# Kernel tuning notes

Hardware: AMD Instinct MI355X
Metric: run time of the kernel (lower is better)

Reference implementation:

```python
import jax, jax.numpy as jnp
import numpy as np

N = 50000      # nodes
E = 800000     # edges (avg degree 16)
IN = 512       # input_dim
R = 128        # feat_reduce_dim
F = 64         # hid_dim per head
H = 4          # n_heads
OUT = 64       # output_dim
ALPHA = 0.2    # leaky_relu slope


def setup_inputs() -> dict:
    key = jax.random.key(0)
    ks = jax.random.split(key, 12)
    x = jax.random.normal(ks[0], (N, IN), dtype=jnp.float32)
    edges = jax.random.randint(ks[1], (2, E), 0, N, dtype=jnp.int32)
    # per-head GAT layer params (fan-in scaled so exp(logits) stays finite)
    W_lin_h = jax.random.normal(ks[2], (H, R, IN), dtype=jnp.float32) * (IN ** -0.5)
    W_seq_h = jax.random.normal(ks[3], (H, F, R), dtype=jnp.float32) * (R ** -0.5)
    a1_h = jax.random.normal(ks[4], (H, F), dtype=jnp.float32) * (F ** -0.5)
    b1_h = jnp.zeros((H,), dtype=jnp.float32)
    a2_h = jax.random.normal(ks[5], (H, F), dtype=jnp.float32) * (F ** -0.5)
    b2_h = jnp.zeros((H,), dtype=jnp.float32)
    bias_h = jnp.zeros((H, F), dtype=jnp.float32)
    # classifier GAT layer (in = H*F = 256, out = OUT)
    W_lin_c = jax.random.normal(ks[6], (R, H * F), dtype=jnp.float32) * ((H * F) ** -0.5)
    W_seq_c = jax.random.normal(ks[7], (OUT, R), dtype=jnp.float32) * (R ** -0.5)
    a1_c = jax.random.normal(ks[8], (OUT,), dtype=jnp.float32) * (OUT ** -0.5)
    b1_c = jnp.zeros((), dtype=jnp.float32)
    a2_c = jax.random.normal(ks[9], (OUT,), dtype=jnp.float32) * (OUT ** -0.5)
    b2_c = jnp.zeros((), dtype=jnp.float32)
    bias_c = jnp.zeros((OUT,), dtype=jnp.float32)
    return dict(x=x, edges=edges, W_lin_h=W_lin_h, W_seq_h=W_seq_h, a1_h=a1_h,
                b1_h=b1_h, a2_h=a2_h, b2_h=b2_h, bias_h=bias_h,
                W_lin_c=W_lin_c, W_seq_c=W_seq_c, a1_c=a1_c, b1_c=b1_c,
                a2_c=a2_c, b2_c=b2_c, bias_c=bias_c)


def _gat_layer(x, src, dst, W_lin, W_seq, a1, b1, a2, b2, bias, concat):
    n = x.shape[0]
    h = x @ W_lin.T                    # [N, R]   (Linear, no bias)
    s = h @ W_seq.T                    # [N, F]   (Conv1d k=1 == matmul)
    f1 = s @ a1 + b1                   # [N]      (f_1 conv)
    f2 = s @ a2 + b2                   # [N]      (f_2 conv)
    logits = f1[src] + f2[dst]         # [E]  edge-gather
    coefs = jnp.exp(jax.nn.leaky_relu(logits, ALPHA))          # [E]
    denom = jax.ops.segment_sum(coefs, src, num_segments=n)    # [N]
    agg = jax.ops.segment_sum(coefs[:, None] * s[dst], src, num_segments=n)  # [N, F]
    ret = agg / denom[:, None] + bias
    return jax.nn.elu(ret) if concat else ret


def reference(x, edges, W_lin_h, W_seq_h, a1_h, b1_h, a2_h, b2_h, bias_h,
              W_lin_c, W_seq_c, a1_c, b1_c, a2_c, b2_c, bias_c):
    src, dst = edges[0], edges[1]
    # n_heads attention layers (concat=True), vmapped over the head axis
    heads = jax.vmap(
        lambda Wl, Ws, a1, b1, a2, b2, b: _gat_layer(
            x, src, dst, Wl, Ws, a1, b1, a2, b2, b, True)
    )(W_lin_h, W_seq_h, a1_h, b1_h, a2_h, b2_h, bias_h)        # [H, N, F]
    hcat = jnp.transpose(heads, (1, 0, 2)).reshape(x.shape[0], -1)  # [N, H*F]
    # classifier GAT layer (concat=False -> no ELU)
    out = _gat_layer(hcat, src, dst, W_lin_c, W_seq_c, a1_c, b1_c,
                     a2_c, b2_c, bias_c, False)                # [N, OUT]
    return out
```

## Files before the change

### kernel.cpp

```cpp
#include <hip/hip_runtime.h>
#include <hip/hip_bf16.h>
#include <cstddef>
#include <cstdint>

#define IN_DIM 512
#define R_DIM 128
#define F_DIM 64
#define H_NUM 4
#define OUT_DIM 64
#define HF 256

typedef __attribute__((ext_vector_type(4))) float f32x4;
typedef __attribute__((ext_vector_type(8))) short bf16x8;

typedef const __attribute__((address_space(1))) void gas_void;
typedef __attribute__((address_space(3))) void las_void;

__device__ __forceinline__ float bf2f(ushort u) {
    union { uint i; float f; } v; v.i = ((uint)u) << 16; return v.f;
}
__device__ __forceinline__ ushort f2bf(float f) {
    union { float f; uint i; } v; v.f = f;
    uint r = v.i + 0x7fff + ((v.i >> 16) & 1);
    return (ushort)(r >> 16);
}
__device__ __forceinline__ float u2f(uint u) {
    union { uint i; float f; } v; v.i = u; return v.f;
}

__global__ __launch_bounds__(256) void zero_i32(int* __restrict__ p, int n) {
    int i = blockIdx.x * 256 + threadIdx.x;
    if (i < n) p[i] = 0;
}

__global__ __launch_bounds__(256) void wcomb_kernel(const float* __restrict__ WlinH,
                                                    const float* __restrict__ WseqH,
                                                    const float* __restrict__ WlinC,
                                                    const float* __restrict__ WseqC,
                                                    ushort* __restrict__ Wc1,
                                                    ushort* __restrict__ Wc2) {
    int idx = blockIdx.x * 256 + threadIdx.x;
    if (idx < H_NUM * F_DIM * IN_DIM) {
        int i  = idx & (IN_DIM - 1);
        int hf = idx >> 9;
        int h  = hf >> 6;
        const float* ws = WseqH + (size_t)hf * R_DIM;
        const float* wl = WlinH + (size_t)h * R_DIM * IN_DIM + i;
        float acc = 0.0f;
#pragma unroll 8
        for (int r = 0; r < R_DIM; ++r) acc += ws[r] * wl[(size_t)r * IN_DIM];
        Wc1[idx] = f2bf(acc);
    } else {
        int idx2 = idx - H_NUM * F_DIM * IN_DIM;
        if (idx2 >= OUT_DIM * HF) return;
        int j = idx2 & (HF - 1);
        int o = idx2 >> 8;
        const float* ws = WseqC + (size_t)o * R_DIM;
        const float* wl = WlinC + j;
        float acc = 0.0f;
#pragma unroll 8
        for (int r = 0; r < R_DIM; ++r) acc += ws[r] * wl[(size_t)r * HF];
        Wc2[idx2] = f2bf(acc);
    }
}

template<int BN, int K, int FS>
__global__ __launch_bounds__(256) void gemm_f32a(const float* __restrict__ A,
                                                 const ushort* __restrict__ B,
                                                 ushort* __restrict__ C,
                                                 int M, int Ntot,
                                                 const float* __restrict__ a1,
                                                 const float* __restrict__ b1,
                                                 const float* __restrict__ a2,
                                                 const float* __restrict__ b2,
                                                 float* __restrict__ f1o,
                                                 float* __restrict__ f2o) {
    constexpr int NF = BN / 16;
    constexpr int HH = BN / 64;
    __shared__ ushort As[64 * 64];
    __shared__ ushort Bs[BN * 64];
    const int tid = threadIdx.x;
    const int wave = tid >> 6;
    const int lane = tid & 63;
    const int lr = lane & 15;
    const int lg = lane >> 4;

    const int b = blockIdx.x;
    const int by = (b >> 3) & 1;
    const int bx = (b >> 4) * 8 + (b & 7);
    const int nbx = (M + 63) >> 6;
    if (bx >= nbx) return;
    const int m0 = bx * 64;
    const int n0 = by * BN;
    const int h0 = by * HH;

    int base[2];
#pragma unroll
    for (int ks = 0; ks < 2; ++ks)
        base[ks] = lr * 128 + (((ks * 4 + lg) ^ (lr & 7)) * 16);
    const int abase0 = wave * 2048 + base[0];
    const int abase1 = wave * 2048 + base[1];

    int s_grow[2], s_ldsoff[2], s_goff[2];
#pragma unroll
    for (int r = 0; r < 2; ++r) {
        int off = r * 4096 + tid * 16;
        int row = off >> 7;
        int lchunk = (off >> 4) & 7;
        int grow = m0 + row;
        if (grow >= M) grow = M - 1;
        s_grow[r] = grow;
        s_goff[r] = lchunk * 8;
        s_ldsoff[r] = row * 128 + ((lchunk ^ (row & 7)) * 16);
    }

    f32x4 acc[NF];
#pragma unroll
    for (int cb = 0; cb < NF; ++cb) acc[cb] = (f32x4)0.0f;

    for (int k0 = 0; k0 < K; k0 += 64) {
#pragma unroll
        for (int r = 0; r < BN / 32; ++r) {
            int off = r * 4096 + tid * 16;
            int row = off >> 7;
            int kch = ((off >> 4) & 7) ^ (row & 7);
            const ushort* g = B + (size_t)(n0 + row) * K + k0 + kch * 8;
            __builtin_amdgcn_global_load_lds((gas_void*)g,
                                             (las_void*)((char*)Bs + off), 16, 0, 0);
        }
#pragma unroll
        for (int r = 0; r < 2; ++r) {
            const float* g = A + (size_t)s_grow[r] * K + k0 + s_goff[r];
            float4 v0 = *(const float4*)(g);
            float4 v1 = *(const float4*)(g + 4);
            ushort us[8] = {f2bf(v0.x), f2bf(v0.y), f2bf(v0.z), f2bf(v0.w),
                            f2bf(v1.x), f2bf(v1.y), f2bf(v1.z), f2bf(v1.w)};
            *(uint4*)((char*)As + s_ldsoff[r]) = *(const uint4*)us;
        }
        __syncthreads();
        {
            bf16x8 af0 = *(const bf16x8*)((const char*)As + abase0);
            bf16x8 af1 = *(const bf16x8*)((const char*)As + abase1);
#pragma unroll
            for (int cg = 0; cg < NF / 4; ++cg) {
                bf16x8 bfr[4];
#pragma unroll
                for (int j = 0; j < 4; ++j)
                    bfr[j] = *(const bf16x8*)((const char*)Bs + (cg * 4 + j) * 2048 + base[0]);
#pragma unroll
                for (int j = 0; j < 4; ++j)
                    acc[cg * 4 + j] = __builtin_amdgcn_mfma_f32_16x16x32_bf16(
                        af0, bfr[j], acc[cg * 4 + j], 0, 0, 0);
#pragma unroll
                for (int j = 0; j < 4; ++j)
                    bfr[j] = *(const bf16x8*)((const char*)Bs + (cg * 4 + j) * 2048 + base[1]);
#pragma unroll
                for (int j = 0; j < 4; ++j)
                    acc[cg * 4 + j] = __builtin_amdgcn_mfma_f32_16x16x32_bf16(
                        af1, bfr[j], acc[cg * 4 + j], 0, 0, 0);
            }
        }
        __syncthreads();
    }

    float a1v[NF], a2v[NF];
#pragma unroll
    for (int cb = 0; cb < NF; ++cb) {
        int col = n0 + cb * 16 + lr;
        a1v[cb] = a1[col];
        a2v[cb] = a2[col];
    }
    const int rowb = m0 + wave * 16 + lg * 4;
#pragma unroll
    for (int r = 0; r < 4; ++r) {
        int row = rowb + r;
        bool ok = row < M;
#pragma unroll
        for (int hh = 0; hh < HH; ++hh) {
            float p1 = 0.f, p2 = 0.f;
#pragma unroll
            for (int c4 = 0; c4 < 4; ++c4) {
                int cb = hh * 4 + c4;
                float v = acc[cb][r];
                p1 += v * a1v[cb];
                p2 += v * a2v[cb];
                if (ok) C[(size_t)row * Ntot + n0 + cb * 16 + lr] = f2bf(v);
            }
#pragma unroll
            for (int m = 1; m < 16; m <<= 1) {
                p1 += __shfl_xor(p1, m, 64);
                p2 += __shfl_xor(p2, m, 64);
            }
            if (lr == 0 && ok) {
                f1o[(size_t)row * FS + h0 + hh] = p1 + b1[h0 + hh];
                f2o[(size_t)row * FS + h0 + hh] = p2 + b2[h0 + hh];
            }
        }
    }
}

template<int BN, int K, int FS>
__global__ __launch_bounds__(256) void gemm_bf16(const ushort* __restrict__ A,
                                                 const ushort* __restrict__ B,
                                                 ushort* __restrict__ C,
                                                 int M, int Ntot,
                                                 const float* __restrict__ a1,
                                                 const float* __restrict__ b1,
                                                 const float* __restrict__ a2,
                                                 const float* __restrict__ b2,
                                                 float* __restrict__ f1o,
                                                 float* __restrict__ f2o) {
    constexpr int NF = BN / 16;
    constexpr int HH = BN / 64;
    __shared__ ushort As[64 * 64];
    __shared__ ushort Bs[BN * 64];
    const int tid = threadIdx.x;
    const int wave = tid >> 6;
    const int lane = tid & 63;
    const int lr = lane & 15;
    const int lg = lane >> 4;
    const int m0 = blockIdx.x * 64;

    int base[2];
#pragma unroll
    for (int ks = 0; ks < 2; ++ks)
        base[ks] = lr * 128 + (((ks * 4 + lg) ^ (lr & 7)) * 16);
    const int abase0 = wave * 2048 + base[0];
    const int abase1 = wave * 2048 + base[1];

    f32x4 acc[NF];
#pragma unroll
    for (int cb = 0; cb < NF; ++cb) acc[cb] = (f32x4)0.0f;

    for (int k0 = 0; k0 < K; k0 += 64) {
#pragma unroll
        for (int r = 0; r < 2; ++r) {
            int off = r * 4096 + tid * 16;
            int row = off >> 7;
            int kch = ((off >> 4) & 7) ^ (row & 7);
            const ushort* g = A + (size_t)(m0 + row) * K + k0 + kch * 8;
            __builtin_amdgcn_global_load_lds((gas_void*)g,
                                             (las_void*)((char*)As + off), 16, 0, 0);
        }
#pragma unroll
        for (int r = 0; r < BN / 32; ++r) {
            int off = r * 4096 + tid * 16;
            int row = off >> 7;
            int kch = ((off >> 4) & 7) ^ (row & 7);
            const ushort* g = B + (size_t)row * K + k0 + kch * 8;
            __builtin_amdgcn_global_load_lds((gas_void*)g,
                                             (las_void*)((char*)Bs + off), 16, 0, 0);
        }
        __syncthreads();
        {
            bf16x8 af0 = *(const bf16x8*)((const char*)As + abase0);
            bf16x8 af1 = *(const bf16x8*)((const char*)As + abase1);
#pragma unroll
            for (int cg = 0; cg < NF / 4; ++cg) {
                bf16x8 bfr[4];
#pragma unroll
                for (int j = 0; j < 4; ++j)
                    bfr[j] = *(const bf16x8*)((const char*)Bs + (cg * 4 + j) * 2048 + base[0]);
#pragma unroll
                for (int j = 0; j < 4; ++j)
                    acc[cg * 4 + j] = __builtin_amdgcn_mfma_f32_16x16x32_bf16(
                        af0, bfr[j], acc[cg * 4 + j], 0, 0, 0);
#pragma unroll
                for (int j = 0; j < 4; ++j)
                    bfr[j] = *(const bf16x8*)((const char*)Bs + (cg * 4 + j) * 2048 + base[1]);
#pragma unroll
                for (int j = 0; j < 4; ++j)
                    acc[cg * 4 + j] = __builtin_amdgcn_mfma_f32_16x16x32_bf16(
                        af1, bfr[j], acc[cg * 4 + j], 0, 0, 0);
            }
        }
        __syncthreads();
    }

    float a1v[NF], a2v[NF];
#pragma unroll
    for (int cb = 0; cb < NF; ++cb) {
        int col = cb * 16 + lr;
        a1v[cb] = a1[col];
        a2v[cb] = a2[col];
    }
    const int rowb = m0 + wave * 16 + lg * 4;
#pragma unroll
    for (int r = 0; r < 4; ++r) {
        int row = rowb + r;
        bool ok = row < M;
#pragma unroll
        for (int hh = 0; hh < HH; ++hh) {
            float p1 = 0.f, p2 = 0.f;
#pragma unroll
            for (int c4 = 0; c4 < 4; ++c4) {
                int cb = hh * 4 + c4;
                float v = acc[cb][r];
                p1 += v * a1v[cb];
                p2 += v * a2v[cb];
                if (ok) C[(size_t)row * Ntot + cb * 16 + lr] = f2bf(v);
            }
#pragma unroll
            for (int m = 1; m < 16; m <<= 1) {
                p1 += __shfl_xor(p1, m, 64);
                p2 += __shfl_xor(p2, m, 64);
            }
            if (lr == 0 && ok) {
                f1o[(size_t)row * FS + hh] = p1 + b1[hh];
                f2o[(size_t)row * FS + hh] = p2 + b2[hh];
            }
        }
    }
}

__global__ __launch_bounds__(256) void hist_kernel(const int* __restrict__ src,
                                                   int* __restrict__ counts, int E) {
    int e = blockIdx.x * 256 + threadIdx.x;
    if (e < E) atomicAdd(&counts[src[e]], 1);
}

__global__ __launch_bounds__(256) void scan_blk(const int* __restrict__ counts,
                                                int* __restrict__ lexcl,
                                                int* __restrict__ part, int N) {
    __shared__ int wsum[4];
    int t = threadIdx.x;
    int g = blockIdx.x * 256 + t;
    int lane = t & 63, wid = t >> 6;
    int v = (g < N) ? counts[g] : 0;
    int x = v;
#pragma unroll
    for (int off = 1; off < 64; off <<= 1) {
        int u = __shfl_up(x, off, 64);
        if (lane >= off) x += u;
    }
    if (lane == 63) wsum[wid] = x;
    __syncthreads();
    int woff = 0;
#pragma unroll
    for (int w = 0; w < 3; ++w) if (w < wid) woff += wsum[w];
    int incl = x + woff;
    if (g < N) lexcl[g] = incl - v;
    if (t == 255) part[blockIdx.x] = incl;
}

__global__ __launch_bounds__(256) void scan_part(int* __restrict__ part, int nb) {
    __shared__ int wsum[4];
    int t = threadIdx.x;
    int lane = t & 63, wid = t >> 6;
    int v = (t < nb) ? part[t] : 0;
    int x = v;
#pragma unroll
    for (int off = 1; off < 64; off <<= 1) {
        int u = __shfl_up(x, off, 64);
        if (lane >= off) x += u;
    }
    if (lane == 63) wsum[wid] = x;
    __syncthreads();
    int woff = 0;
#pragma unroll
    for (int w = 0; w < 3; ++w) if (w < wid) woff += wsum[w];
    int incl = x + woff;
    __syncthreads();
    if (t < nb) part[t] = incl - v;
    if (t == 255) part[nb] = incl;
}

__global__ __launch_bounds__(256) void scan_add(const int* __restrict__ lexcl,
                                                const int* __restrict__ part,
                                                int* __restrict__ starts,
                                                int* __restrict__ cursor, int N, int nb) {
    int g = blockIdx.x * 256 + threadIdx.x;
    if (g < N) {
        int s = lexcl[g] + part[blockIdx.x];
        starts[g] = s;
        cursor[g] = s;
    }
    if (g == 0) starts[N] = part[nb];
}

__global__ __launch_bounds__(256) void scatter_kernel(const int* __restrict__ src,
                                                      const int* __restrict__ dst,
                                                      int* __restrict__ cursor,
                                                      int* __restrict__ dsts, int E) {
    int e = blockIdx.x * 256 + threadIdx.x;
    if (e >= E) return;
    int p = atomicAdd(&cursor[src[e]], 1);
    dsts[p] = dst[e];
}

__global__ __launch_bounds__(256) void gather1_kernel(const int* __restrict__ starts,
                                                      const int* __restrict__ dsts,
                                                      const float* __restrict__ f1,
                                                      const float* __restrict__ f2,
                                                      const ushort* __restrict__ S1,
                                                      const float* __restrict__ bias,
                                                      ushort* __restrict__ hcat, int N) {
    int n = (int)((blockIdx.x * blockDim.x + threadIdx.x) >> 6);
    int lane = threadIdx.x & 63;
    if (n >= N) return;
    const int es = lane >> 5;
    const int fl = lane & 31;
    const int head = fl >> 3;
    const float f1h = f1[(size_t)n * 4 + head];
    int beg = starts[n], end = starts[n + 1];
    float a[8] = {};
    float den = 0.f;
    int i = beg;

#define G1_EDGE(D)                                                            \
    {                                                                         \
        float g_ = f2[(size_t)(D) * 4 + head];                                \
        uint4 r_ = *(const uint4*)(S1 + (size_t)(D) * HF + fl * 8);           \
        float l_ = f1h + g_; l_ = l_ > 0.f ? l_ : 0.2f * l_;                  \
        float c_ = __expf(l_);                                                \
        a[0] += c_ * u2f(r_.x << 16);  a[1] += c_ * u2f(r_.x & 0xffff0000u);  \
        a[2] += c_ * u2f(r_.y << 16);  a[3] += c_ * u2f(r_.y & 0xffff0000u);  \
        a[4] += c_ * u2f(r_.z << 16);  a[5] += c_ * u2f(r_.z & 0xffff0000u);  \
        a[6] += c_ * u2f(r_.w << 16);  a[7] += c_ * u2f(r_.w & 0xffff0000u);  \
        den += c_;                                                            \
    }

    for (; i + 4 <= end; i += 4) {
        int dA = dsts[i + es];
        int dB = dsts[i + 2 + es];
        G1_EDGE(dA);
        G1_EDGE(dB);
    }
    if (i + 2 <= end) {
        int d = dsts[i + es];
        G1_EDGE(d);
        i += 2;
    }
    if (i < end && es == 0) {
        int d = dsts[i];
        G1_EDGE(d);
    }
#undef G1_EDGE

#pragma unroll
    for (int k = 0; k < 8; ++k) a[k] += __shfl_xor(a[k], 32, 64);
    den += __shfl_xor(den, 32, 64);

    if (es == 0) {
        float rd = __builtin_amdgcn_rcpf(den);
        float4 b0 = *(const float4*)(bias + fl * 8);
        float4 b1 = *(const float4*)(bias + fl * 8 + 4);
        float v[8];
        v[0] = a[0] * rd + b0.x; v[1] = a[1] * rd + b0.y;
        v[2] = a[2] * rd + b0.z; v[3] = a[3] * rd + b0.w;
        v[4] = a[4] * rd + b1.x; v[5] = a[5] * rd + b1.y;
        v[6] = a[6] * rd + b1.z; v[7] = a[7] * rd + b1.w;
        ushort us[8];
#pragma unroll
        for (int k = 0; k < 8; ++k) {
            float vv = v[k] > 0.f ? v[k] : __expf(v[k]) - 1.f;
            us[k] = f2bf(vv);
        }
        *(uint4*)(hcat + (size_t)n * HF + fl * 8) = *(const uint4*)us;
    }
}

__global__ __launch_bounds__(256) void gather2_kernel(const int* __restrict__ starts,
                                                      const int* __restrict__ dsts,
                                                      const float* __restrict__ f1,
                                                      const float* __restrict__ f2,
                                                      const ushort* __restrict__ S2,
                                                      const float* __restrict__ bias,
                                                      float* __restrict__ out, int N) {
    int n = (int)((blockIdx.x * blockDim.x + threadIdx.x) >> 6);
    int lane = threadIdx.x & 63;
    if (n >= N) return;
    const int es = lane >> 5;
    const int fl = lane & 31;
    const float f1u = f1[n];
    int beg = starts[n], end = starts[n + 1];
    float a0 = 0.f, a1 = 0.f, den = 0.f;
    int i = beg;

#define G2_EDGE(D)                                                            \
    {                                                                         \
        float g_ = f2[(D)];                                                   \
        uint r_ = *(const uint*)(S2 + (size_t)(D) * OUT_DIM + fl * 2);        \
        float l_ = f1u + g_; l_ = l_ > 0.f ? l_ : 0.2f * l_;                  \
        float c_ = __expf(l_);                                                \
        a0 += c_ * u2f(r_ << 16);                                             \
        a1 += c_ * u2f(r_ & 0xffff0000u);                                     \
        den += c_;                                                            \
    }

    for (; i + 4 <= end; i += 4) {
        int dA = dsts[i + es];
        int dB = dsts[i + 2 + es];
        G2_EDGE(dA);
        G2_EDGE(dB);
    }
    if (i + 2 <= end) {
        int d = dsts[i + es];
        G2_EDGE(d);
        i += 2;
    }
    if (i < end && es == 0) {
        int d = dsts[i];
        G2_EDGE(d);
    }
#undef G2_EDGE

    a0 += __shfl_xor(a0, 32, 64);
    a1 += __shfl_xor(a1, 32, 64);
    den += __shfl_xor(den, 32, 64);

    if (es == 0) {
        float rd = __builtin_amdgcn_rcpf(den);
        float2 b = *(const float2*)(bias + fl * 2);
        float2 o;
        o.x = a0 * rd + b.x;
        o.y = a1 * rd + b.y;
        *(float2*)(out + (size_t)n * OUT_DIM + fl * 2) = o;
    }
}

extern "C" void kernel_launch(void* const* d_in, const int* in_sizes, int n_in,
                              void* d_out, int out_size, void* d_ws, size_t ws_size,
                              hipStream_t stream) {
    const float* x      = (const float*)d_in[0];
    const int*   edges  = (const int*)d_in[1];
    const float* Wlin_h = (const float*)d_in[2];
    const float* Wseq_h = (const float*)d_in[3];
    const float* a1_h   = (const float*)d_in[4];
    const float* b1_h   = (const float*)d_in[5];
    const float* a2_h   = (const float*)d_in[6];
    const float* b2_h   = (const float*)d_in[7];
    const float* bias_h = (const float*)d_in[8];
    const float* Wlin_c = (const float*)d_in[9];
    const float* Wseq_c = (const float*)d_in[10];
    const float* a1_c   = (const float*)d_in[11];
    const float* b1_c   = (const float*)d_in[12];
    const float* a2_c   = (const float*)d_in[13];
    const float* b2_c   = (const float*)d_in[14];
    const float* bias_c = (const float*)d_in[15];

    const int N = in_sizes[0] / IN_DIM;
    const int E = in_sizes[1] / 2;
    const int* src = edges;
    const int* dst = edges + E;

    char* ws = (char*)d_ws;
    size_t off = 0;
    ushort* WC1   = (ushort*)(ws + off); off += (size_t)HF * IN_DIM * 2;
    ushort* WC2   = (ushort*)(ws + off); off += (size_t)OUT_DIM * HF * 2;
    ushort* S1    = (ushort*)(ws + off); off += (size_t)N * HF * 2;
    ushort* S2    = S1;
    ushort* HCAT  = (ushort*)(ws + off); off += (size_t)N * HF * 2;
    float*  F1    = (float*)(ws + off);  off += (size_t)N * H_NUM * 4;
    float*  F2    = (float*)(ws + off);  off += (size_t)N * H_NUM * 4;
    float*  F1c   = (float*)(ws + off);  off += (size_t)N * 4;
    float*  F2c   = (float*)(ws + off);  off += (size_t)N * 4;
    int* COUNTS   = (int*)(ws + off);    off += (size_t)N * 4;
    int* STARTS   = (int*)(ws + off);    off += ((size_t)N + 1) * 4;
    int* CURSOR   = (int*)(ws + off);    off += (size_t)N * 4;
    int* DSTS     = (int*)(ws + off);    off += (size_t)E * 4;
    int* LEXCL    = (int*)(ws + off);    off += (size_t)N * 4;
    int* PART     = (int*)(ws + off);    off += 512 * 4;

    float* out = (float*)d_out;

    const int eg = (E + 255) / 256;
    const int NB = (N + 255) / 256;

    hipLaunchKernelGGL(zero_i32, dim3(NB), dim3(256), 0, stream, COUNTS, N);
    hipLaunchKernelGGL(hist_kernel, dim3(eg), dim3(256), 0, stream, src, COUNTS, E);
    hipLaunchKernelGGL(scan_blk, dim3(NB), dim3(256), 0, stream, COUNTS, LEXCL, PART, N);
    hipLaunchKernelGGL(scan_part, dim3(1), dim3(256), 0, stream, PART, NB);
    hipLaunchKernelGGL(scan_add, dim3(NB), dim3(256), 0, stream, LEXCL, PART, STARTS, CURSOR, N, NB);
    hipLaunchKernelGGL(scatter_kernel, dim3(eg), dim3(256), 0, stream, src, dst, CURSOR, DSTS, E);

    hipLaunchKernelGGL(wcomb_kernel,
                       dim3((H_NUM * F_DIM * IN_DIM + OUT_DIM * HF + 255) / 256), dim3(256),
                       0, stream, Wlin_h, Wseq_h, Wlin_c, Wseq_c, WC1, WC2);

    {
        int nbx = (N + 63) / 64;
        int gx = 16 * ((nbx + 7) / 8);
        hipLaunchKernelGGL((gemm_f32a<128, IN_DIM, 4>), dim3(gx), dim3(256),
                           0, stream, x, WC1, S1, N, HF,
                           a1_h, b1_h, a2_h, b2_h, F1, F2);
    }

    hipLaunchKernelGGL(gather1_kernel, dim3((N + 3) / 4), dim3(256), 0, stream,
                       STARTS, DSTS, F1, F2, S1, bias_h, HCAT, N);

    hipLaunchKernelGGL((gemm_bf16<OUT_DIM, HF, 1>), dim3((N + 63) / 64, 1), dim3(256),
                       0, stream, HCAT, WC2, S2, N, OUT_DIM,
                       a1_c, b1_c, a2_c, b2_c, F1c, F2c);

    hipLaunchKernelGGL(gather2_kernel, dim3((N + 3) / 4), dim3(256), 0, stream,
                       STARTS, DSTS, F1c, F2c, S2, bias_c, out, N);
}
```

Baseline: 248.1 us.

## Shrink first GEMM M-tile to 32 rows with 2x2 wave grid

The fp32-input GEMM now uses 32-row tiles instead of 64, arranging the four waves as 2 row groups by 2 head-column groups, so each wave holds 4 accumulator fragments instead of 8. This doubles the number of blocks, which should raise occupancy and parallelism and reduce register pressure. The cost is that each B tile loaded into LDS is reused across half as many rows, so total B traffic doubles. The per-head f1/f2 reduction is reassigned so each wave computes one head.

After: 243.7 us. About the same (-1.8%).

```diff
diff --git a/kernel.cpp b/kernel.cpp
--- a/kernel.cpp
+++ b/kernel.cpp
@@ -75,44 +75,39 @@
                                                  const float* __restrict__ b2,
                                                  float* __restrict__ f1o,
                                                  float* __restrict__ f2o) {
-    constexpr int NF = BN / 16;
-    constexpr int HH = BN / 64;
-    __shared__ ushort As[64 * 64];
+    constexpr int NF = 4;
+    __shared__ ushort As[32 * 64];
     __shared__ ushort Bs[BN * 64];
     const int tid = threadIdx.x;
     const int wave = tid >> 6;
     const int lane = tid & 63;
     const int lr = lane & 15;
     const int lg = lane >> 4;
+    const int wr = wave & 1;
+    const int wc = wave >> 1;
 
     const int b = blockIdx.x;
     const int by = (b >> 3) & 1;
     const int bx = (b >> 4) * 8 + (b & 7);
-    const int nbx = (M + 63) >> 6;
+    const int nbx = (M + 31) >> 5;
     if (bx >= nbx) return;
-    const int m0 = bx * 64;
+    const int m0 = bx * 32;
     const int n0 = by * BN;
-    const int h0 = by * HH;
+    const int h0 = by * 2;
 
     int base[2];
 #pragma unroll
     for (int ks = 0; ks < 2; ++ks)
         base[ks] = lr * 128 + (((ks * 4 + lg) ^ (lr & 7)) * 16);
-    const int abase0 = wave * 2048 + base[0];
-    const int abase1 = wave * 2048 + base[1];
-
-    int s_grow[2], s_ldsoff[2], s_goff[2];
-#pragma unroll
-    for (int r = 0; r < 2; ++r) {
-        int off = r * 4096 + tid * 16;
-        int row = off >> 7;
-        int lchunk = (off >> 4) & 7;
-        int grow = m0 + row;
-        if (grow >= M) grow = M - 1;
-        s_grow[r] = grow;
-        s_goff[r] = lchunk * 8;
-        s_ldsoff[r] = row * 128 + ((lchunk ^ (row & 7)) * 16);
-    }
+    const int abase0 = wr * 2048 + base[0];
+    const int abase1 = wr * 2048 + base[1];
+
+    const int s_row = tid >> 3;
+    const int s_lchunk = tid & 7;
+    int s_grow = m0 + s_row;
+    if (s_grow >= M) s_grow = M - 1;
+    const int s_ldsoff = s_row * 128 + ((s_lchunk ^ (s_row & 7)) * 16);
+    const int s_goff = s_lchunk * 8;
 
     f32x4 acc[NF];
 #pragma unroll
@@ -128,73 +123,66 @@
             __builtin_amdgcn_global_load_lds((gas_void*)g,
                                              (las_void*)((char*)Bs + off), 16, 0, 0);
         }
-#pragma unroll
-        for (int r = 0; r < 2; ++r) {
-            const float* g = A + (size_t)s_grow[r] * K + k0 + s_goff[r];
+        {
+            const float* g = A + (size_t)s_grow * K + k0 + s_goff;
             float4 v0 = *(const float4*)(g);
             float4 v1 = *(const float4*)(g + 4);
             ushort us[8] = {f2bf(v0.x), f2bf(v0.y), f2bf(v0.z), f2bf(v0.w),
                             f2bf(v1.x), f2bf(v1.y), f2bf(v1.z), f2bf(v1.w)};
-            *(uint4*)((char*)As + s_ldsoff[r]) = *(const uint4*)us;
+            *(uint4*)((char*)As + s_ldsoff) = *(const uint4*)us;
         }
         __syncthreads();
         {
             bf16x8 af0 = *(const bf16x8*)((const char*)As + abase0);
             bf16x8 af1 = *(const bf16x8*)((const char*)As + abase1);
-#pragma unroll
-            for (int cg = 0; cg < NF / 4; ++cg) {
-                bf16x8 bfr[4];
-#pragma unroll
-                for (int j = 0; j < 4; ++j)
-                    bfr[j] = *(const bf16x8*)((const char*)Bs + (cg * 4 + j) * 2048 + base[0]);
-#pragma unroll
-                for (int j = 0; j < 4; ++j)
-                    acc[cg * 4 + j] = __builtin_amdgcn_mfma_f32_16x16x32_bf16(
-                        af0, bfr[j], acc[cg * 4 + j], 0, 0, 0);
-#pragma unroll
-                for (int j = 0; j < 4; ++j)
-                    bfr[j] = *(const bf16x8*)((const char*)Bs + (cg * 4 + j) * 2048 + base[1]);
-#pragma unroll
-                for (int j = 0; j < 4; ++j)
-                    acc[cg * 4 + j] = __builtin_amdgcn_mfma_f32_16x16x32_bf16(
-                        af1, bfr[j], acc[cg * 4 + j], 0, 0, 0);
-            }
+            bf16x8 bfr[NF];
+#pragma unroll
+            for (int j = 0; j < NF; ++j)
+                bfr[j] = *(const bf16x8*)((const char*)Bs + (wc * 4 + j) * 2048 + base[0]);
+#pragma unroll
+            for (int j = 0; j < NF; ++j)
+                acc[j] = __builtin_amdgcn_mfma_f32_16x16x32_bf16(
+                    af0, bfr[j], acc[j], 0, 0, 0);
+#pragma unroll
+            for (int j = 0; j < NF; ++j)
+                bfr[j] = *(const bf16x8*)((const char*)Bs + (wc * 4 + j) * 2048 + base[1]);
+#pragma unroll
+            for (int j = 0; j < NF; ++j)
+                acc[j] = __builtin_amdgcn_mfma_f32_16x16x32_bf16(
+                    af1, bfr[j], acc[j], 0, 0, 0);
         }
         __syncthreads();
     }
 
+    const int head = h0 + wc;
     float a1v[NF], a2v[NF];
 #pragma unroll
     for (int cb = 0; cb < NF; ++cb) {
-        int col = n0 + cb * 16 + lr;
+        int col = n0 + wc * 64 + cb * 16 + lr;
         a1v[cb] = a1[col];
         a2v[cb] = a2[col];
     }
-    const int rowb = m0 + wave * 16 + lg * 4;
+    const int rowb = m0 + wr * 16 + lg * 4;
 #pragma unroll
     for (int r = 0; r < 4; ++r) {
         int row = rowb + r;
         bool ok = row < M;
-#pragma unroll
-        for (int hh = 0; hh < HH; ++hh) {
-            float p1 = 0.f, p2 = 0.f;
-#pragma unroll
-            for (int c4 = 0; c4 < 4; ++c4) {
-                int cb = hh * 4 + c4;
-                float v = acc[cb][r];
-                p1 += v * a1v[cb];
-                p2 += v * a2v[cb];
-                if (ok) C[(size_t)row * Ntot + n0 + cb * 16 + lr] = f2bf(v);
-            }
-#pragma unroll
-            for (int m = 1; m < 16; m <<= 1) {
-                p1 += __shfl_xor(p1, m, 64);
-                p2 += __shfl_xor(p2, m, 64);
-            }
-            if (lr == 0 && ok) {
-                f1o[(size_t)row * FS + h0 + hh] = p1 + b1[h0 + hh];
-                f2o[(size_t)row * FS + h0 + hh] = p2 + b2[h0 + hh];
-            }
+        float p1 = 0.f, p2 = 0.f;
+#pragma unroll
+        for (int cb = 0; cb < NF; ++cb) {
+            float v = acc[cb][r];
+            p1 += v * a1v[cb];
+            p2 += v * a2v[cb];
+            if (ok) C[(size_t)row * Ntot + n0 + wc * 64 + cb * 16 + lr] = f2bf(v);
+        }
+#pragma unroll
+        for (int m = 1; m < 16; m <<= 1) {
+            p1 += __shfl_xor(p1, m, 64);
+            p2 += __shfl_xor(p2, m, 64);
+        }
+        if (lr == 0 && ok) {
+            f1o[(size_t)row * FS + head] = p1 + b1[head];
+            f2o[(size_t)row * FS + head] = p2 + b2[head];
         }
     }
 }
@@ -579,7 +567,7 @@
                        0, stream, Wlin_h, Wseq_h, Wlin_c, Wseq_c, WC1, WC2);
 
     {
-        int nbx = (N + 63) / 64;
+        int nbx = (N + 31) / 32;
         int gx = 16 * ((nbx + 7) / 8);
         hipLaunchKernelGGL((gemm_f32a<128, IN_DIM, 4>), dim3(gx), dim3(256),
                            0, stream, x, WC1, S1, N, HF,
```
